# Optimization experiments

Hardware: AMD Instinct MI355X
Metric: run time of the kernel (lower is better)

Reference implementation:

```python
import jax, jax.numpy as jnp
import numpy as np

B = 256; L = 512; PRED = 96; DVARS = 21
P = 16; STRIDE = 16
N = (L - P) // STRIDE + 1      # 32 patches
DM = P * P                     # d_model = 256
K = 5                          # DctAtt low-freq coeffs
EPS_BN = 1e-5


def _dct_mats(n_len):
    # torch_dct DCT-II / DCT-III as dense matrices (exact same scaling as torch_dct)
    n = jnp.arange(n_len, dtype=jnp.float32)
    C = jnp.cos(jnp.pi * (2.0 * n[None, :] + 1.0) * n[:, None] / (2.0 * n_len))  # (k, m)
    D2 = 2.0 * C                                  # dct(x, norm=None):  X = x @ D2.T
    w0 = jnp.where(n == 0, 0.5, 1.0)
    D3 = (C.T * w0[None, :]) / n_len              # idct(X, norm=None): x = X @ D3.T
    rL = jnp.sqrt(jnp.asarray(n_len, jnp.float32))
    s_ortho = jnp.where(n == 0, 0.5 / rL, 0.5 * jnp.sqrt(2.0) / rL)  # unnorm -> ortho scale
    return D2, D3, s_ortho


def _bn(x, g, b):
    # BatchNorm1d, training-mode batch stats (biased var), x: (B, C, Lc)
    m = jnp.mean(x, axis=(0, 2), keepdims=True)
    v = jnp.var(x, axis=(0, 2), keepdims=True)
    return g[None, :, None] * (x - m) * jax.lax.rsqrt(v + EPS_BN) + b[None, :, None]


def _gelu(x):
    return jax.nn.gelu(x, approximate=False)  # torch nn.GELU default = exact erf


def setup_inputs():
    key = jax.random.key(0)
    ks = jax.random.split(key, 24)
    r = lambda i, shp, s=0.02: jax.random.normal(ks[i], shp, jnp.float32) * s
    return dict(
        x=jax.random.normal(ks[0], (B, L, DVARS), jnp.float32),
        w_dct=r(1, (DVARS,), 0.2), b_dct=r(2, (DVARS,), 0.02),
        W_embed=r(3, (P, DM), 0.05), b_embed=r(4, (DM,), 0.02),
        W_linres=r(5, (N * DM, PRED), 0.01), b_linres=r(6, (PRED,), 0.02),
        W_dres=r(7, (DM, P), 0.05), b_dres=r(8, (P,), 0.02),
        w_dc=r(9, (N, P), 0.1), b_dc=r(10, (N,), 0.02),
        w_dc1=r(11, (N, 3), 0.2), b_dc1=r(12, (N,), 0.02),
        g_dctnorm=jnp.ones((DVARS,), jnp.float32), b_dctnorm=jnp.zeros((DVARS,), jnp.float32),
        g_patchnorm=jnp.ones((N,), jnp.float32), b_patchnorm=jnp.zeros((N,), jnp.float32),
        g_depthnorm=jnp.ones((N,), jnp.float32), b_depthnorm=jnp.zeros((N,), jnp.float32),
        thr_p=jnp.array([0.3], jnp.float32),
        W_m1=r(13, (L, PRED), 0.02), b_m1=r(14, (PRED,), 0.02),
        W_m2=r(15, (PRED, PRED), 0.05), b_m2=r(16, (PRED,), 0.02),
        a_dw_w=r(17, (K,), 0.2), a_dw_b=r(18, (), 0.02),
        a_cw=jnp.float32(1.0) + r(19, (), 0.1), a_cb=r(20, (), 0.02),
        a_g=jnp.ones((), jnp.float32), a_b=jnp.zeros((), jnp.float32),
    )


def reference(x, w_dct, b_dct, W_embed, b_embed, W_linres, b_linres,
              W_dres, b_dres, w_dc, b_dc, w_dc1, b_dc1,
              g_dctnorm, b_dctnorm, g_patchnorm, b_patchnorm,
              g_depthnorm, b_depthnorm, thr_p,
              W_m1, b_m1, W_m2, b_m2,
              a_dw_w, a_dw_b, a_cw, a_cb, a_g, a_b):
    Bx = x.shape[0]
    D2, D3, s_ortho = _dct_mats(L)
    xT = jnp.transpose(x, (0, 2, 1))                       # (B,D,L)
    # dctConv = depthwise 1x1 conv => per-channel scale+bias (same layer reused twice)
    x_res = xT * w_dct[:, None] + b_dct[:, None]
    z_dct = xT @ D2.T                                      # dct(norm=None)
    # adaptive_high_freq_mask
    energy = jnp.sum(z_dct * z_dct, axis=-1)               # (B,D)
    med = jnp.median(energy, axis=1, keepdims=True)
    norm_e = energy / (med + 1e-6)
    thr = jnp.quantile(norm_e, thr_p[0])                   # global quantile over all elems
    mask = (norm_e > thr).astype(x.dtype)[..., None]       # broadcasts over freq axis
    z = (z_dct * mask) * w_dct[:, None] + b_dct[:, None]
    z = _gelu(z)
    z = _bn(z, g_dctnorm, b_dctnorm)
    z1 = z @ D3.T + x_res                                  # idct + residual, (B,D,L)
    # patchify (unfold)
    idx = jnp.arange(N)[:, None] * STRIDE + jnp.arange(P)[None, :]
    zp = xT[..., idx].reshape(Bx * DVARS, N, P)            # (BD,N,P)
    z_p = zp @ W_embed + b_embed                           # (BD,N,DM)
    z_res = jnp.transpose(z_p.reshape(Bx, DVARS, N * DM) @ W_linres + b_linres, (0, 2, 1))
    res = z_p @ W_dres + b_dres                            # (BD,N,P)
    # depth_conv: depthwise conv, kernel=P, stride=P over DM=P*P
    zd = jnp.einsum('bnqp,np->bnq', z_p.reshape(Bx * DVARS, N, P, P), w_dc) + b_dc[:, None]
    zd = _bn(zd + res, g_patchnorm, b_patchnorm)
    z2 = _gelu(zd)
    # depth_conv1: depthwise k=3 pad=1
    zpad = jnp.pad(z2, ((0, 0), (0, 0), (1, 1)))
    zc = (w_dc1[:, 0, None] * zpad[..., :-2] + w_dc1[:, 1, None] * zpad[..., 1:-1]
          + w_dc1[:, 2, None] * zpad[..., 2:]) + b_dc1[:, None]
    zc = _bn(zc, g_depthnorm, b_depthnorm)
    zc = _gelu(zc) + z2
    z2f = zc.reshape(Bx, DVARS, N * P)                     # (B,D,L)
    # DctAtt on z1*z2f (low-freq pick + dwConv(k=5,stride=5) + BN(1) + GELU + 1x1 + softmax)
    prod = z1 * z2f
    low = (prod @ D2.T[:, :K]) * s_ortho[:K]               # ortho DCT, first K coeffs (B,D,K)
    att = low @ a_dw_w + a_dw_b                            # (B,D)
    m = jnp.mean(att); v = jnp.var(att)
    att = a_g * (att - m) * jax.lax.rsqrt(v + EPS_BN) + a_b
    att = _gelu(att)
    att1 = jax.nn.softmax(att * a_cw + a_cb, axis=-1)[..., None]  # (B,D,1)
    zsum = z1 * att1 + z2f * (1.0 - att1)
    z_mlp = _gelu(zsum @ W_m1 + b_m1) @ W_m2 + b_m2        # Mlp, (B,D,PRED)
    return z_res + jnp.transpose(z_mlp, (0, 2, 1))         # (B,PRED,D)
```

## Files before the change

### kernel.cpp

```cpp
#include <hip/hip_runtime.h>
#include <hip/hip_bf16.h>

#define B_    256
#define L_    512
#define DV    21
#define NROW  5376
#define NP    32
#define PP    16
#define PRED_ 96

static const size_t OFF_XT    = 0;
static const size_t OFF_ZA    = 2752512;
static const size_t OFF_Z1    = 5505024;
static const size_t OFF_ZCP   = 8257536;
static const size_t OFF_D2    = 11010048;
static const size_t OFF_D3    = 11272192;
static const size_t OFF_M     = 11534336;
static const size_t OFF_TN    = 11583488;
static const size_t OFF_TB    = 11591680;
static const size_t OFF_C     = 11592192;
static const size_t OFF_EN    = 11592320;
static const size_t OFF_NORM  = 11597696;
static const size_t OFF_ATT   = 11603072;
static const size_t OFF_ATT1  = 11608448;
static const size_t OFF_STAT  = 11613824;
static const size_t OFF_ABD   = 11614080;
static const size_t OFF_ABP   = 11614144;
static const size_t OFF_ABDEP = 11614208;
static const size_t OFF_FLAG  = 11614272;
static const size_t OFF_STG   = 11614336;

static const int S_WDCT=0, S_BDCT=24, S_WE=48, S_BE=4144, S_WL=4400, S_BL=790832,
  S_WD=790928, S_BDRES=795024, S_WDC=795040, S_BDC=795552, S_WDC1=795584, S_BDC1=795680,
  S_GD=795712, S_BDN=795736, S_GP=795760, S_BP=795792, S_GDEP=795824, S_BDEP=795856,
  S_THR=795888, S_WM1=795892, S_BM1=845044, S_WM2=845140, S_BM2=854356,
  S_ADWW=854452, S_ADWB=854460, S_ACW=854464, S_ACB=854468, S_AG=854472, S_AB2=854476;

struct Ptrs { const void* p[30]; };

typedef __attribute__((ext_vector_type(8))) short bf16x8;
typedef __attribute__((ext_vector_type(4))) float f32x4;

__device__ __forceinline__ float bf2f(unsigned short h){
  unsigned u = ((unsigned)h) << 16;
  return __uint_as_float(u);
}
__device__ __forceinline__ short f2b(float f){
  unsigned u = __float_as_uint(f);
  u = (u + 0x7FFFu + ((u >> 16) & 1u)) >> 16;
  return (short)u;
}
__device__ __forceinline__ float gelu_f(float x){ return 0.5f*x*(1.0f+erff(x*0.70710678118654752440f)); }

__global__ void k_init(const unsigned* __restrict__ gones, float* __restrict__ stat,
                       float* __restrict__ c, float* __restrict__ M, int* __restrict__ flag){
  if (blockIdx.x == 0){
    stat[threadIdx.x] = 0.0f;
    if (threadIdx.x < 128) c[threadIdx.x] = 0.0f;
    if (threadIdx.x == 0) *flag = (gones[0] == 0x3F800000u) ? 1 : 0;
  } else {
    M[(blockIdx.x-1)*256 + threadIdx.x] = 0.0f;
  }
}

__global__ __launch_bounds__(256) void k_stage(Ptrs ptrs, float* __restrict__ dst, const int* __restrict__ flag){
  const int cnt[29] = {21,21,4096,256,786432,96,4096,16,512,32,96,32,21,21,32,32,32,32,1,49152,96,9216,96,5,1,1,1,1,1};
  const int off[29] = {S_WDCT,S_BDCT,S_WE,S_BE,S_WL,S_BL,S_WD,S_BDRES,S_WDC,S_BDC,S_WDC1,S_BDC1,
                       S_GD,S_BDN,S_GP,S_BP,S_GDEP,S_BDEP,S_THR,S_WM1,S_BM1,S_WM2,S_BM2,
                       S_ADWW,S_ADWB,S_ACW,S_ACB,S_AG,S_AB2};
  int mode = *flag;
  int gid = blockIdx.x*256 + threadIdx.x;
  int a = -1, loc = 0, base = 0;
  #pragma unroll
  for (int i = 0; i < 29; i++){
    if (a < 0 && gid < base + cnt[i]){ a = i; loc = gid - base; }
    base += cnt[i];
  }
  if (a < 0) return;
  const void* s = ptrs.p[a+1];
  float v = mode ? ((const float*)s)[loc] : bf2f(((const unsigned short*)s)[loc]);
  dst[off[a] + loc] = v;
}

__global__ __launch_bounds__(256) void k_transpose(const void* __restrict__ x, float* __restrict__ xt,
                                                   const int* __restrict__ flag){
  __shared__ float xs[128*DV];
  int mode = *flag;
  int b = blockIdx.x >> 2, ch = blockIdx.x & 3;
  int l0 = ch*128;
  size_t base = (size_t)b*(L_*DV) + (size_t)l0*DV;
  if (mode){
    const float* xp = (const float*)x + base;
    for (int i = threadIdx.x; i < 128*DV; i += 256) xs[i] = xp[i];
  } else {
    const unsigned short* xp = (const unsigned short*)x + base;
    for (int i = threadIdx.x; i < 128*DV; i += 256) xs[i] = bf2f(xp[i]);
  }
  __syncthreads();
  for (int i = threadIdx.x; i < 128*DV; i += 256){
    int d = i >> 7, l = i & 127;
    xt[((size_t)b*DV + d)*512 + l0 + l] = xs[l*DV + d];
  }
}

__global__ __launch_bounds__(256) void k_dctmats(float* __restrict__ D2, unsigned short* __restrict__ D3h){
  int i = blockIdx.x*256 + threadIdx.x;
  int kk = i >> 9, m = i & 511;
  const float PIo = 3.14159265358979323846f / 1024.0f;
  int a = ((2*m+1)*kk) & 2047;
  D2[i] = 2.0f * cosf(PIo * (float)a);
  int l = kk, k = m;
  int a2 = ((2*l+1)*k) & 2047;
  float w0 = (k==0) ? 0.5f : 1.0f;
  D3h[i] = (unsigned short)f2b(cosf(PIo * (float)a2) * w0 * (1.0f/512.0f));
}

__global__ void k_dvec(const float* __restrict__ S, float* __restrict__ dvec){
  int m = blockIdx.x*256 + threadIdx.x;
  const float PIo = 3.14159265358979323846f / 1024.0f;
  const float rs = 22.627416997969522f;
  float s = 0.f;
  #pragma unroll
  for (int k = 0; k < 5; k++){
    float sk = ((k == 0) ? 0.5f : 0.70710678118654752440f) / rs;
    int a = ((2*m+1)*k) & 2047;
    s += 2.0f * cosf(PIo * (float)a) * sk * S[S_ADWW + k];
  }
  dvec[m] = s;
}

__global__ __launch_bounds__(256) void k_foldM(const float* __restrict__ S, float* __restrict__ M){
  const float* We = S + S_WE;  const float* Wl = S + S_WL;
  int gid = blockIdx.x*256 + threadIdx.x;
  int l = gid/96, p = gid - l*96;
  int n = l>>4, q = l&15;
  int j0 = blockIdx.y*32;
  float acc = 0.f;
  #pragma unroll 8
  for (int j = j0; j < j0+32; j++) acc += We[q*256+j] * Wl[(size_t)(n*256+j)*96 + p];
  atomicAdd(&M[gid], acc);
}

__global__ __launch_bounds__(256) void k_foldC(const float* __restrict__ S, float* __restrict__ c){
  const float* be = S + S_BE;  const float* Wl = S + S_WL;  const float* bl = S + S_BL;
  int t = threadIdx.x;
  int rp = t >> 7, p = t & 127;
  if (p >= 96) return;
  float acc = 0.f;
  int J0 = blockIdx.x*64;
  for (int j = 0; j < 64; j += 2){
    int J = J0 + j + rp;
    acc += be[J & 255] * Wl[(size_t)J*96 + p];
  }
  if (blockIdx.x == 0 && rp == 0) acc += bl[p];
  atomicAdd(&c[p], acc);
}

__global__ __launch_bounds__(256) void k_foldTn(const float* __restrict__ S,
    float* __restrict__ Tn, float* __restrict__ tb){
  __shared__ float WeS[4096];
  __shared__ float WdS[4096];
  __shared__ float wdcS[16];
  __shared__ float beS[256];
  __shared__ float bdresS[16];
  int n = blockIdx.x, tid = threadIdx.x;
  for (int i = tid; i < 4096; i += 256){ WeS[i] = S[S_WE+i]; WdS[i] = S[S_WD+i]; }
  beS[tid & 255] = S[S_BE + (tid & 255)];
  if (tid < 16){ wdcS[tid] = S[S_WDC + n*16 + tid]; bdresS[tid] = S[S_BDRES + tid]; }
  __syncthreads();
  int q2 = tid>>4, q = tid&15;
  float R = 0.f;
  for (int j = 0; j < 256; j++) R += WeS[q2*256+j] * WdS[j*16+q];
  float G = 0.f;
  #pragma unroll
  for (int p = 0; p < 16; p++) G += WeS[q2*256 + q*16 + p] * wdcS[p];
  Tn[n*256 + q2*16 + q] = R + G;
  if (tid < 16){
    float rb = bdresS[tid];
    for (int j = 0; j < 256; j++) rb += beS[j] * WdS[j*16+tid];
    float gb = S[S_BDC + n];
    #pragma unroll
    for (int p = 0; p < 16; p++) gb += beS[tid*16+p] * wdcS[p];
    tb[n*16+tid] = rb + gb;
  }
}

__global__ __launch_bounds__(256) void k_gemm0(
    const float* __restrict__ A, const float* __restrict__ Bm, float* __restrict__ C){
  __shared__ float As[16][68];
  __shared__ float Bs[16][68];
  int tid = threadIdx.x;
  int tx = tid & 15, ty = tid >> 4;
  int rowBase = blockIdx.y * 64;
  int colBase = blockIdx.x * 64;
  int lr = tid >> 2;
  int lk = (tid & 3) << 2;
  float acc[4][4] = {};
  for (int k0 = 0; k0 < 512; k0 += 16){
    float4 av = *(const float4*)(A + (size_t)(rowBase+lr)*512 + k0 + lk);
    As[lk+0][lr] = av.x; As[lk+1][lr] = av.y; As[lk+2][lr] = av.z; As[lk+3][lr] = av.w;
    float4 bv = *(const float4*)(Bm + (size_t)(colBase+lr)*512 + k0 + lk);
    Bs[lk+0][lr] = bv.x; Bs[lk+1][lr] = bv.y; Bs[lk+2][lr] = bv.z; Bs[lk+3][lr] = bv.w;
    __syncthreads();
    #pragma unroll
    for (int kk = 0; kk < 16; kk++){
      float4 a4 = *(const float4*)&As[kk][ty*4];
      float4 b4 = *(const float4*)&Bs[kk][tx*4];
      acc[0][0] += a4.x*b4.x; acc[0][1] += a4.x*b4.y; acc[0][2] += a4.x*b4.z; acc[0][3] += a4.x*b4.w;
      acc[1][0] += a4.y*b4.x; acc[1][1] += a4.y*b4.y; acc[1][2] += a4.y*b4.z; acc[1][3] += a4.y*b4.w;
      acc[2][0] += a4.z*b4.x; acc[2][1] += a4.z*b4.y; acc[2][2] += a4.z*b4.z; acc[2][3] += a4.z*b4.w;
      acc[3][0] += a4.w*b4.x; acc[3][1] += a4.w*b4.y; acc[3][2] += a4.w*b4.z; acc[3][3] += a4.w*b4.w;
    }
    __syncthreads();
  }
  #pragma unroll
  for (int i = 0; i < 4; i++){
    int r = rowBase + ty*4 + i;
    #pragma unroll
    for (int j = 0; j < 4; j++){
      int cc = colBase + tx*4 + j;
      C[(size_t)r*512 + cc] = acc[i][j];
    }
  }
}

template<int MODE>
__global__ __launch_bounds__(256) void k_gemm_mf(
    const float* __restrict__ A, const float* __restrict__ A2,
    const unsigned short* __restrict__ Bg,
    float* __restrict__ C, const float* __restrict__ ab, const float* __restrict__ xt,
    const float* __restrict__ wdct, const float* __restrict__ bdct, int Cstride){
  __shared__ short Ah[64*40];
  __shared__ short Bh[64*40];
  int tid = threadIdx.x;
  int rowBase = blockIdx.y*64, colBase = blockIdx.x*64;
  int srow = tid>>2, seg = tid&3;
  int r = rowBase + srow;
  float alpha = 1.f, beta = 0.f;
  bool useXt = false;
  if (MODE == 1){ int d = r % DV; alpha = ab[2*d]; beta = ab[2*d+1]; }
  if (MODE == 3){ if (blockIdx.x < 2) alpha = ab[r]; else useXt = true; }
  int wave = tid>>6, lane = tid&63;
  int m = lane&15, quad = lane>>4;
  f32x4 acc[4] = {};
  const float* Ap = (MODE == 3 && useXt) ? xt : A;
  for (int k0 = 0; k0 < 512; k0 += 32){
    float4 a0 = *(const float4*)(Ap + (size_t)r*512 + k0 + seg*8);
    float4 a1 = *(const float4*)(Ap + (size_t)r*512 + k0 + seg*8 + 4);
    if (MODE == 1){
      a0.x = alpha*a0.x+beta; a0.y = alpha*a0.y+beta; a0.z = alpha*a0.z+beta; a0.w = alpha*a0.w+beta;
      a1.x = alpha*a1.x+beta; a1.y = alpha*a1.y+beta; a1.z = alpha*a1.z+beta; a1.w = alpha*a1.w+beta;
    }
    if (MODE == 3 && !useXt){
      float4 c0 = *(const float4*)(A2 + (size_t)r*512 + k0 + seg*8);
      float4 c1 = *(const float4*)(A2 + (size_t)r*512 + k0 + seg*8 + 4);
      float om = 1.0f - alpha;
      a0.x = alpha*a0.x + om*c0.x; a0.y = alpha*a0.y + om*c0.y;
      a0.z = alpha*a0.z + om*c0.z; a0.w = alpha*a0.w + om*c0.w;
      a1.x = alpha*a1.x + om*c1.x; a1.y = alpha*a1.y + om*c1.y;
      a1.z = alpha*a1.z + om*c1.z; a1.w = alpha*a1.w + om*c1.w;
    }
    bf16x8 av;
    av[0]=f2b(a0.x); av[1]=f2b(a0.y); av[2]=f2b(a0.z); av[3]=f2b(a0.w);
    av[4]=f2b(a1.x); av[5]=f2b(a1.y); av[6]=f2b(a1.z); av[7]=f2b(a1.w);
    *(bf16x8*)(Ah + srow*40 + seg*8) = av;
    bf16x8 bv = *(const bf16x8*)(Bg + (size_t)(colBase+srow)*512 + k0 + seg*8);
    *(bf16x8*)(Bh + srow*40 + seg*8) = bv;
    __syncthreads();
    bf16x8 af = *(bf16x8*)(Ah + (wave*16 + m)*40 + quad*8);
    #pragma unroll
    for (int t = 0; t < 4; t++){
      bf16x8 bf = *(bf16x8*)(Bh + (t*16 + m)*40 + quad*8);
      acc[t] = __builtin_amdgcn_mfma_f32_16x16x32_bf16(af, bf, acc[t], 0, 0, 0);
    }
    __syncthreads();
  }
  #pragma unroll
  for (int t = 0; t < 4; t++){
    #pragma unroll
    for (int i = 0; i < 4; i++){
      int rr = rowBase + wave*16 + quad*4 + i;
      int cc = colBase + t*16 + m;
      float v = acc[t][i];
      if (MODE == 1){
        int d = rr % DV;
        v += xt[(size_t)rr*512 + cc]*wdct[d] + bdct[d];
      }
      C[(size_t)rr*Cstride + cc] = v;
    }
  }
}

__global__ __launch_bounds__(256) void k_energy(const float* __restrict__ z, float* __restrict__ e){
  int tid = threadIdx.x;
  int r = blockIdx.x*4 + (tid>>6);
  int lane = tid & 63;
  const float* p = z + (size_t)r*512;
  float s = 0.f;
  #pragma unroll
  for (int w = 0; w < 8; w++){ float v = p[lane + w*64]; s += v*v; }
  for (int off = 32; off; off >>= 1) s += __shfl_down(s, off);
  if (lane == 0) e[r] = s;
}

__global__ __launch_bounds__(256) void k_med(const float* __restrict__ e, float* __restrict__ norm){
  int b = threadIdx.x;
  float v[DV];
  for (int d = 0; d < DV; d++) v[d] = e[b*DV + d];
  float med = 0.f;
  for (int i = 0; i < DV; i++){
    int rk = 0;
    for (int j = 0; j < DV; j++) rk += (v[j] < v[i]) || (v[j] == v[i] && j < i);
    if (rk == 10) med = v[i];
  }
  float den = med + 1e-6f;
  for (int d = 0; d < DV; d++) norm[b*DV + d] = v[d] / den;
}

__global__ __launch_bounds__(256) void k_rank(const float* __restrict__ norm,
    const float* __restrict__ thrv, float* __restrict__ stat){
  int tid = threadIdx.x;
  int cand = tid >> 4, part = tid & 15;
  int idx = blockIdx.x*16 + cand;
  float val = norm[idx];
  int cnt = 0;
  int j0 = part*336;
  for (int j = j0; j < j0 + 336; ++j){
    float v = norm[j];
    cnt += (v < val) || (v == val && j < idx);
  }
  __shared__ int sc[16][17];
  sc[cand][part] = cnt;
  __syncthreads();
  if (part == 0){
    int rank = 0;
    #pragma unroll
    for (int i = 0; i < 16; i++) rank += sc[cand][i];
    float q = thrv[0];
    float pos = q * 5375.0f;
    int i0 = (int)floorf(pos);
    int i1 = (i0 + 1 > 5375) ? 5375 : i0 + 1;
    if (rank == i0) stat[200] = val;
    if (rank == i1) stat[201] = val;
  }
}

__global__ __launch_bounds__(256) void k_maskgelu(float* __restrict__ zA, const float* __restrict__ norm,
    const float* __restrict__ stat, const float* __restrict__ thrv,
    const float* __restrict__ wdct, const float* __restrict__ bdct,
    float* __restrict__ part){
  int r = blockIdx.x, tid = threadIdx.x;
  int d = r % DV, brow = r / DV;
  float q = thrv[0];
  float pos = q * 5375.0f; float f = pos - floorf(pos);
  float thr = stat[200] + (stat[201] - stat[200]) * f;
  float mask = norm[r] > thr ? 1.0f : 0.0f;
  float w = wdct[d], b = bdct[d];
  float s = 0.f, s2 = 0.f;
  for (int i = tid; i < 512; i += 256){
    float v = zA[(size_t)r*512 + i] * mask * w + b;
    float g = gelu_f(v);
    zA[(size_t)r*512 + i] = g;
    s += g; s2 += g*g;
  }
  for (int off = 32; off; off >>= 1){ s += __shfl_down(s, off); s2 += __shfl_down(s2, off); }
  __shared__ float wsum[4][2];
  int wv = tid >> 6;
  if ((tid & 63) == 0){ wsum[wv][0] = s; wsum[wv][1] = s2; }
  __syncthreads();
  if (tid == 0){
    float S  = wsum[0][0]+wsum[1][0]+wsum[2][0]+wsum[3][0];
    float S2 = wsum[0][1]+wsum[1][1]+wsum[2][1]+wsum[3][1];
    part[(2*d)*256 + brow] = S;
    part[(2*d+1)*256 + brow] = S2;
  }
}

__global__ __launch_bounds__(256) void k_bnfin2(const float* __restrict__ part, int P,
    const float* __restrict__ g, const float* __restrict__ b, float count, float* __restrict__ ab){
  int c = blockIdx.x, tid = threadIdx.x;
  const float* ps = part + (size_t)(2*c)*P;
  const float* pq = part + (size_t)(2*c+1)*P;
  float s = 0.f, s2 = 0.f;
  for (int i = tid; i < P; i += 256){ s += ps[i]; s2 += pq[i]; }
  for (int off = 32; off; off >>= 1){ s += __shfl_down(s, off); s2 += __shfl_down(s2, off); }
  __shared__ float ws[4][2];
  if ((tid & 63) == 0){ ws[tid>>6][0] = s; ws[tid>>6][1] = s2; }
  __syncthreads();
  if (tid == 0){
    float S1 = ws[0][0]+ws[1][0]+ws[2][0]+ws[3][0];
    float S2 = ws[0][1]+ws[1][1]+ws[2][1]+ws[3][1];
    float mean = S1 / count;
    float var  = S2 / count - mean*mean;
    float al = g[c] * rsqrtf(var + 1e-5f);
    float be = b[c] - mean * al;
    ab[2*c] = al; ab[2*c+1] = be;
  }
}

__global__ __launch_bounds__(256) void k_patch(const float* __restrict__ xt, const float* __restrict__ Tn,
    const float* __restrict__ tb, float* __restrict__ t, float* __restrict__ part){
  int blk = blockIdx.x, tid = threadIdx.x;
  int n0 = tid >> 4, qq = tid & 15;
  int n1 = n0 + 16;
  float T0[16], T1[16];
  #pragma unroll
  for (int q2 = 0; q2 < 16; q2++){
    T0[q2] = Tn[n0*256 + q2*16 + qq];
    T1[q2] = Tn[n1*256 + q2*16 + qq];
  }
  float tb0 = tb[n0*16 + qq], tb1 = tb[n1*16 + qq];
  float s0 = 0.f, q0 = 0.f, s1 = 0.f, q1 = 0.f;
  #pragma unroll
  for (int rr = 0; rr < 4; rr++){
    int r = blk*4 + rr;
    float x0 = xt[(size_t)r*512 + tid];
    float x1 = xt[(size_t)r*512 + tid + 256];
    float a0 = tb0, a1 = tb1;
    #pragma unroll
    for (int q2 = 0; q2 < 16; q2++){
      a0 += __shfl(x0, q2, 16) * T0[q2];
      a1 += __shfl(x1, q2, 16) * T1[q2];
    }
    t[(size_t)r*512 + tid] = a0;       s0 += a0; q0 += a0*a0;
    t[(size_t)r*512 + tid + 256] = a1; s1 += a1; q1 += a1*a1;
  }
  #pragma unroll
  for (int off = 1; off < 16; off <<= 1){
    s0 += __shfl_xor(s0, off); q0 += __shfl_xor(q0, off);
    s1 += __shfl_xor(s1, off); q1 += __shfl_xor(q1, off);
  }
  if (qq == 0){
    part[(2*n0)*1344 + blk] = s0; part[(2*n0+1)*1344 + blk] = q0;
    part[(2*n1)*1344 + blk] = s1; part[(2*n1+1)*1344 + blk] = q1;
  }
}

__global__ __launch_bounds__(256) void k_z2(float* __restrict__ t, float* __restrict__ zcp,
    const float* __restrict__ abp, const float* __restrict__ wdc1,
    const float* __restrict__ bdc1, float* __restrict__ part){
  int blk = blockIdx.x, tid = threadIdx.x;
  int n0 = tid >> 4, qq = tid & 15;
  int n1 = n0 + 16;
  float al0 = abp[2*n0], be0 = abp[2*n0+1], al1 = abp[2*n1], be1 = abp[2*n1+1];
  float w00 = wdc1[n0*3], w01 = wdc1[n0*3+1], w02 = wdc1[n0*3+2], bb0 = bdc1[n0];
  float w10 = wdc1[n1*3], w11 = wdc1[n1*3+1], w12 = wdc1[n1*3+2], bb1 = bdc1[n1];
  float s0 = 0.f, q0 = 0.f, s1 = 0.f, q1 = 0.f;
  #pragma unroll
  for (int rr = 0; rr < 4; rr++){
    int r = blk*4 + rr;
    float v0 = t[(size_t)r*512 + tid];
    float v1 = t[(size_t)r*512 + tid + 256];
    float z0  = gelu_f(al0*v0 + be0);
    float z1v = gelu_f(al1*v1 + be1);
    float l0 = __shfl_up(z0, 1, 16);    if (qq == 0)  l0 = 0.f;
    float r0 = __shfl_down(z0, 1, 16);  if (qq == 15) r0 = 0.f;
    float l1 = __shfl_up(z1v, 1, 16);   if (qq == 0)  l1 = 0.f;
    float r1 = __shfl_down(z1v, 1, 16); if (qq == 15) r1 = 0.f;
    float cv0 = w00*l0 + w01*z0  + w02*r0 + bb0;
    float cv1 = w10*l1 + w11*z1v + w12*r1 + bb1;
    zcp[(size_t)r*512 + tid] = cv0;       t[(size_t)r*512 + tid] = z0;
    zcp[(size_t)r*512 + tid + 256] = cv1; t[(size_t)r*512 + tid + 256] = z1v;
    s0 += cv0; q0 += cv0*cv0; s1 += cv1; q1 += cv1*cv1;
  }
  #pragma unroll
  for (int off = 1; off < 16; off <<= 1){
    s0 += __shfl_xor(s0, off); q0 += __shfl_xor(q0, off);
    s1 += __shfl_xor(s1, off); q1 += __shfl_xor(q1, off);
  }
  if (qq == 0){
    part[(2*n0)*1344 + blk] = s0; part[(2*n0+1)*1344 + blk] = q0;
    part[(2*n1)*1344 + blk] = s1; part[(2*n1+1)*1344 + blk] = q1;
  }
}

__global__ __launch_bounds__(256) void k_z2fatt(float* __restrict__ zcp, const float* __restrict__ z2,
    const float* __restrict__ ab, const float* __restrict__ z1,
    const float* __restrict__ dvec, float* __restrict__ att){
  int r = blockIdx.x, tid = threadIdx.x;
  size_t base = (size_t)r*512;
  float s = 0.f;
  #pragma unroll
  for (int h = 0; h < 2; h++){
    int idx = tid + h*256;
    int n = (idx >> 4) & 31;
    float v = gelu_f(ab[2*n]*zcp[base+idx] + ab[2*n+1]) + z2[base+idx];
    zcp[base+idx] = v;
    s += z1[base+idx] * v * dvec[idx];
  }
  for (int off = 32; off; off >>= 1) s += __shfl_down(s, off);
  __shared__ float ws[4];
  if ((tid & 63) == 0) ws[tid>>6] = s;
  __syncthreads();
  if (tid == 0) att[r] = ws[0]+ws[1]+ws[2]+ws[3];
}

__global__ __launch_bounds__(256) void k_attfin(const float* __restrict__ att, const float* __restrict__ S,
                                                float* __restrict__ att1){
  __shared__ float ws[4][2];
  int tid = threadIdx.x;
  float s = 0.f, s2 = 0.f;
  for (int i = tid; i < NROW; i += 256){ float a = att[i]; s += a; s2 += a*a; }
  for (int off = 32; off; off >>= 1){ s += __shfl_down(s, off); s2 += __shfl_down(s2, off); }
  if ((tid & 63) == 0){ ws[tid>>6][0] = s; ws[tid>>6][1] = s2; }
  __syncthreads();
  float S1 = ws[0][0]+ws[1][0]+ws[2][0]+ws[3][0];
  float S2 = ws[0][1]+ws[1][1]+ws[2][1]+ws[3][1];
  float mean = S1 / 5376.0f;
  float var  = S2 / 5376.0f - mean*mean;
  float al = S[S_AG] * rsqrtf(var + 1e-5f);
  float bb = S[S_AB2];
  float cw = S[S_ACW], cb2 = S[S_ACB];
  int b = tid;
  float v[DV]; float mx = -1e30f;
  for (int d = 0; d < DV; d++){
    float a = att[b*DV + d];
    a = gelu_f(al*(a - mean) + bb);
    a = a*cw + cb2;
    v[d] = a; mx = fmaxf(mx, a);
  }
  float ss = 0.f;
  for (int d = 0; d < DV; d++){ v[d] = expf(v[d] - mx); ss += v[d]; }
  float inv = 1.0f / ss;
  for (int d = 0; d < DV; d++) att1[b*DV + d] = v[d] * inv;
}

__global__ __launch_bounds__(256) void k_bcat(const float* __restrict__ Wm1, const float* __restrict__ M,
                                              unsigned short* __restrict__ Bt){
  int i = blockIdx.x*256 + threadIdx.x;
  int c = i >> 9, m = i & 511;
  float v = 0.f;
  if (c < 96) v = Wm1[m*96 + c];
  else if (c >= 128 && c < 224) v = M[m*96 + (c - 128)];
  Bt[i] = (unsigned short)f2b(v);
}

__global__ __launch_bounds__(256) void k_out(const float* __restrict__ Hcat, const float* __restrict__ c,
    const float* __restrict__ S, void* __restrict__ outv, const int* __restrict__ flag){
  const float* bm1 = S + S_BM1;
  const float* Wm2 = S + S_WM2;
  const float* bm2 = S + S_BM2;
  __shared__ float W2s[96*96];
  __shared__ float Hs[16][100];
  int blk = blockIdx.x, tid = threadIdx.x;
  int r0 = blk*16;
  for (int i = tid; i < 96*96; i += 256) W2s[i] = Wm2[i];
  for (int i = tid; i < 16*96; i += 256){
    int rr = i / 96, col = i - rr*96;
    Hs[rr][col] = gelu_f(Hcat[(size_t)(r0+rr)*256 + col] + bm1[col]);
  }
  __syncthreads();
  int rr = tid >> 4, c0 = (tid & 15)*6;
  float acc[6] = {};
  for (int k = 0; k < 96; k++){
    float h = Hs[rr][k];
    #pragma unroll
    for (int j = 0; j < 6; j++) acc[j] += h * W2s[k*96 + c0 + j];
  }
  int r = r0 + rr;
  int b = r / DV, d = r - b*DV;
  int mode = *flag;
  #pragma unroll
  for (int j = 0; j < 6; j++){
    int p = c0 + j;
    float val = Hcat[(size_t)r*256 + 128 + p] + c[p] + acc[j] + bm2[p];
    size_t oi = ((size_t)b*96 + p)*DV + d;
    if (mode) ((float*)outv)[oi] = val;
    else ((__hip_bfloat16*)outv)[oi] = __float2bfloat16(val);
  }
}

extern "C" void kernel_launch(void* const* d_in, const int* in_sizes, int n_in,
                              void* d_out, int out_size, void* d_ws, size_t ws_size,
                              hipStream_t stream) {
  float* w = (float*)d_ws;
  float* xt   = w + OFF_XT;
  float* zA   = w + OFF_ZA;
  float* z1   = w + OFF_Z1;
  float* zcp  = w + OFF_ZCP;
  float* D2   = w + OFF_D2;
  unsigned short* D3h = (unsigned short*)(w + OFF_D3);
  float* Mb   = w + OFF_M;
  float* Tn   = w + OFF_TN;
  float* tb   = w + OFF_TB;
  float* cb   = w + OFF_C;
  float* en   = w + OFF_EN;
  float* nrm  = w + OFF_NORM;
  float* att  = w + OFF_ATT;
  float* att1 = w + OFF_ATT1;
  float* dvec = w + OFF_ATT1;
  float* stat = w + OFF_STAT;
  float* abd  = w + OFF_ABD;
  float* abp  = w + OFF_ABP;
  float* abdep= w + OFF_ABDEP;
  int*   flag = (int*)(w + OFF_FLAG);
  float* S    = w + OFF_STG;
  float* Hcat = zA;
  unsigned short* BcatTh = (unsigned short*)(zA + 1500000);
  float* partA = D2;
  float* partB = w + OFF_D3;

  Ptrs ptrs;
  for (int i = 0; i < 30; i++) ptrs.p[i] = d_in[i];

  k_init<<<193, 256, 0, stream>>>((const unsigned*)d_in[13], stat, cb, Mb, flag);
  k_stage<<<3338, 256, 0, stream>>>(ptrs, S, flag);
  k_transpose<<<1024, 256, 0, stream>>>(d_in[0], xt, flag);
  k_dctmats<<<1024, 256, 0, stream>>>(D2, D3h);
  k_dvec<<<2, 256, 0, stream>>>(S, dvec);
  k_foldM<<<dim3(192, 8), 256, 0, stream>>>(S, Mb);
  k_foldC<<<128, 256, 0, stream>>>(S, cb);
  k_foldTn<<<32, 256, 0, stream>>>(S, Tn, tb);

  k_gemm0<<<dim3(8,84), 256, 0, stream>>>(xt, D2, zA);
  k_energy<<<NROW/4, 256, 0, stream>>>(zA, en);
  k_med<<<1, 256, 0, stream>>>(en, nrm);
  k_rank<<<336, 256, 0, stream>>>(nrm, S+S_THR, stat);
  k_maskgelu<<<NROW, 256, 0, stream>>>(zA, nrm, stat, S+S_THR, S+S_WDCT, S+S_BDCT, partA);
  k_bnfin2<<<DV, 256, 0, stream>>>(partA, 256, S+S_GD, S+S_BDN, 131072.0f, abd);
  k_gemm_mf<1><<<dim3(8,84), 256, 0, stream>>>(zA, nullptr, D3h, z1, abd, xt, S+S_WDCT, S+S_BDCT, 512);

  k_patch<<<NROW/4, 256, 0, stream>>>(xt, Tn, tb, zA, partA);
  k_bnfin2<<<NP, 256, 0, stream>>>(partA, 1344, S+S_GP, S+S_BP, 86016.0f, abp);
  k_z2<<<NROW/4, 256, 0, stream>>>(zA, zcp, abp, S+S_WDC1, S+S_BDC1, partB);
  k_bnfin2<<<NP, 256, 0, stream>>>(partB, 1344, S+S_GDEP, S+S_BDEP, 86016.0f, abdep);
  k_z2fatt<<<NROW, 256, 0, stream>>>(zcp, zA, abdep, z1, dvec, att);
  k_attfin<<<1, 256, 0, stream>>>(att, S, att1);

  k_bcat<<<512, 256, 0, stream>>>(S+S_WM1, Mb, BcatTh);
  k_gemm_mf<3><<<dim3(4,84), 256, 0, stream>>>(z1, zcp, BcatTh, Hcat, att1, xt, nullptr, nullptr, 256);
  k_out<<<NROW/16, 256, 0, stream>>>(Hcat, cb, S, d_out, flag);
}
```

Baseline: 348.7 us.

## Run DCT GEMM on bf16 MFMA with hi/lo split and fuse energy reduction

The first DCT GEMM moves from an FP32 scalar-FMA tile loop to bf16 MFMA instructions. Both operands are split into hi and lo bf16 parts and multiplied with four MFMAs per tile to keep close to FP32 accuracy. The per-row energy sum-of-squares is now computed in the GEMM epilogue as per-block partials, reduced by a tiny kernel, which replaces the separate energy pass over zA. The dvec computation is folded into the DCT-matrix kernel to save a launch. The split-bf16 product drops the lo*lo rounding fidelity, so there is a small precision risk, and the workspace buffers are re-aliased.

```diff
diff --git a/kernel.cpp b/kernel.cpp
--- a/kernel.cpp
+++ b/kernel.cpp
@@ -103,30 +103,33 @@
   }
 }
 
-__global__ __launch_bounds__(256) void k_dctmats(float* __restrict__ D2, unsigned short* __restrict__ D3h){
+__global__ __launch_bounds__(256) void k_dctmats(unsigned short* __restrict__ D2h,
+    unsigned short* __restrict__ D2l, unsigned short* __restrict__ D3h,
+    const float* __restrict__ S, float* __restrict__ dvec){
   int i = blockIdx.x*256 + threadIdx.x;
   int kk = i >> 9, m = i & 511;
   const float PIo = 3.14159265358979323846f / 1024.0f;
   int a = ((2*m+1)*kk) & 2047;
-  D2[i] = 2.0f * cosf(PIo * (float)a);
+  float v = 2.0f * cosf(PIo * (float)a);
+  short hi = f2b(v);
+  float lo = v - bf2f((unsigned short)hi);
+  D2h[i] = (unsigned short)hi;
+  D2l[i] = (unsigned short)f2b(lo);
   int l = kk, k = m;
   int a2 = ((2*l+1)*k) & 2047;
   float w0 = (k==0) ? 0.5f : 1.0f;
   D3h[i] = (unsigned short)f2b(cosf(PIo * (float)a2) * w0 * (1.0f/512.0f));
-}
-
-__global__ void k_dvec(const float* __restrict__ S, float* __restrict__ dvec){
-  int m = blockIdx.x*256 + threadIdx.x;
-  const float PIo = 3.14159265358979323846f / 1024.0f;
-  const float rs = 22.627416997969522f;
-  float s = 0.f;
-  #pragma unroll
-  for (int k = 0; k < 5; k++){
-    float sk = ((k == 0) ? 0.5f : 0.70710678118654752440f) / rs;
-    int a = ((2*m+1)*k) & 2047;
-    s += 2.0f * cosf(PIo * (float)a) * sk * S[S_ADWW + k];
-  }
-  dvec[m] = s;
+  if (i < 512){
+    const float rs = 22.627416997969522f;
+    float s = 0.f;
+    #pragma unroll
+    for (int k5 = 0; k5 < 5; k5++){
+      float sk = ((k5 == 0) ? 0.5f : 0.70710678118654752440f) / rs;
+      int a5 = ((2*i+1)*k5) & 2047;
+      s += 2.0f * cosf(PIo * (float)a5) * sk * S[S_ADWW + k5];
+    }
+    dvec[i] = s;
+  }
 }
 
 __global__ __launch_bounds__(256) void k_foldM(const float* __restrict__ S, float* __restrict__ M){
@@ -186,42 +189,83 @@
 }
 
 __global__ __launch_bounds__(256) void k_gemm0(
-    const float* __restrict__ A, const float* __restrict__ Bm, float* __restrict__ C){
-  __shared__ float As[16][68];
-  __shared__ float Bs[16][68];
+    const float* __restrict__ A, const unsigned short* __restrict__ Bh16,
+    const unsigned short* __restrict__ Bl16, float* __restrict__ C,
+    float* __restrict__ e_part){
+  __shared__ short Ahi[64*40];
+  __shared__ short Alo[64*40];
+  __shared__ short Bhi[64*40];
+  __shared__ short Blo[64*40];
   int tid = threadIdx.x;
-  int tx = tid & 15, ty = tid >> 4;
-  int rowBase = blockIdx.y * 64;
-  int colBase = blockIdx.x * 64;
-  int lr = tid >> 2;
-  int lk = (tid & 3) << 2;
-  float acc[4][4] = {};
-  for (int k0 = 0; k0 < 512; k0 += 16){
-    float4 av = *(const float4*)(A + (size_t)(rowBase+lr)*512 + k0 + lk);
-    As[lk+0][lr] = av.x; As[lk+1][lr] = av.y; As[lk+2][lr] = av.z; As[lk+3][lr] = av.w;
-    float4 bv = *(const float4*)(Bm + (size_t)(colBase+lr)*512 + k0 + lk);
-    Bs[lk+0][lr] = bv.x; Bs[lk+1][lr] = bv.y; Bs[lk+2][lr] = bv.z; Bs[lk+3][lr] = bv.w;
+  int rowBase = blockIdx.y*64, colBase = blockIdx.x*64;
+  int srow = tid>>2, seg = tid&3;
+  int r = rowBase + srow;
+  int wave = tid>>6, lane = tid&63;
+  int m = lane&15, quad = lane>>4;
+  f32x4 acc[4] = {};
+  for (int k0 = 0; k0 < 512; k0 += 32){
+    float4 a0 = *(const float4*)(A + (size_t)r*512 + k0 + seg*8);
+    float4 a1 = *(const float4*)(A + (size_t)r*512 + k0 + seg*8 + 4);
+    bf16x8 ah, al;
+    {
+      float av[8] = {a0.x,a0.y,a0.z,a0.w,a1.x,a1.y,a1.z,a1.w};
+      #pragma unroll
+      for (int j = 0; j < 8; j++){
+        short h = f2b(av[j]);
+        ah[j] = h;
+        al[j] = f2b(av[j] - bf2f((unsigned short)h));
+      }
+    }
+    *(bf16x8*)(Ahi + srow*40 + seg*8) = ah;
+    *(bf16x8*)(Alo + srow*40 + seg*8) = al;
+    *(bf16x8*)(Bhi + srow*40 + seg*8) = *(const bf16x8*)(Bh16 + (size_t)(colBase+srow)*512 + k0 + seg*8);
+    *(bf16x8*)(Blo + srow*40 + seg*8) = *(const bf16x8*)(Bl16 + (size_t)(colBase+srow)*512 + k0 + seg*8);
     __syncthreads();
-    #pragma unroll
-    for (int kk = 0; kk < 16; kk++){
-      float4 a4 = *(const float4*)&As[kk][ty*4];
-      float4 b4 = *(const float4*)&Bs[kk][tx*4];
-      acc[0][0] += a4.x*b4.x; acc[0][1] += a4.x*b4.y; acc[0][2] += a4.x*b4.z; acc[0][3] += a4.x*b4.w;
-      acc[1][0] += a4.y*b4.x; acc[1][1] += a4.y*b4.y; acc[1][2] += a4.y*b4.z; acc[1][3] += a4.y*b4.w;
-      acc[2][0] += a4.z*b4.x; acc[2][1] += a4.z*b4.y; acc[2][2] += a4.z*b4.z; acc[2][3] += a4.z*b4.w;
-      acc[3][0] += a4.w*b4.x; acc[3][1] += a4.w*b4.y; acc[3][2] += a4.w*b4.z; acc[3][3] += a4.w*b4.w;
+    bf16x8 afh = *(bf16x8*)(Ahi + (wave*16 + m)*40 + quad*8);
+    bf16x8 afl = *(bf16x8*)(Alo + (wave*16 + m)*40 + quad*8);
+    #pragma unroll
+    for (int t = 0; t < 4; t++){
+      bf16x8 bfh = *(bf16x8*)(Bhi + (t*16 + m)*40 + quad*8);
+      bf16x8 bfl = *(bf16x8*)(Blo + (t*16 + m)*40 + quad*8);
+      acc[t] = __builtin_amdgcn_mfma_f32_16x16x32_bf16(afh, bfh, acc[t], 0, 0, 0);
+      acc[t] = __builtin_amdgcn_mfma_f32_16x16x32_bf16(afh, bfl, acc[t], 0, 0, 0);
+      acc[t] = __builtin_amdgcn_mfma_f32_16x16x32_bf16(afl, bfh, acc[t], 0, 0, 0);
+      acc[t] = __builtin_amdgcn_mfma_f32_16x16x32_bf16(afl, bfl, acc[t], 0, 0, 0);
     }
     __syncthreads();
   }
-  #pragma unroll
-  for (int i = 0; i < 4; i++){
-    int r = rowBase + ty*4 + i;
-    #pragma unroll
-    for (int j = 0; j < 4; j++){
-      int cc = colBase + tx*4 + j;
-      C[(size_t)r*512 + cc] = acc[i][j];
-    }
-  }
+  float es[4] = {};
+  #pragma unroll
+  for (int t = 0; t < 4; t++){
+    #pragma unroll
+    for (int i = 0; i < 4; i++){
+      int rr = rowBase + wave*16 + quad*4 + i;
+      int cc = colBase + t*16 + m;
+      float v = acc[t][i];
+      C[(size_t)rr*512 + cc] = v;
+      es[i] += v*v;
+    }
+  }
+  #pragma unroll
+  for (int off = 1; off < 16; off <<= 1){
+    #pragma unroll
+    for (int i = 0; i < 4; i++) es[i] += __shfl_xor(es[i], off);
+  }
+  if (m == 0){
+    #pragma unroll
+    for (int i = 0; i < 4; i++){
+      int rr = rowBase + wave*16 + quad*4 + i;
+      e_part[rr*8 + blockIdx.x] = es[i];
+    }
+  }
+}
+
+__global__ __launch_bounds__(256) void k_ered(const float* __restrict__ e_part, float* __restrict__ e){
+  int r = blockIdx.x*256 + threadIdx.x;
+  float s = 0.f;
+  #pragma unroll
+  for (int j = 0; j < 8; j++) s += e_part[r*8 + j];
+  e[r] = s;
 }
 
 template<int MODE>
@@ -291,18 +335,6 @@
   }
 }
 
-__global__ __launch_bounds__(256) void k_energy(const float* __restrict__ z, float* __restrict__ e){
-  int tid = threadIdx.x;
-  int r = blockIdx.x*4 + (tid>>6);
-  int lane = tid & 63;
-  const float* p = z + (size_t)r*512;
-  float s = 0.f;
-  #pragma unroll
-  for (int w = 0; w < 8; w++){ float v = p[lane + w*64]; s += v*v; }
-  for (int off = 32; off; off >>= 1) s += __shfl_down(s, off);
-  if (lane == 0) e[r] = s;
-}
-
 __global__ __launch_bounds__(256) void k_med(const float* __restrict__ e, float* __restrict__ norm){
   int b = threadIdx.x;
   float v[DV];
@@ -578,7 +610,8 @@
   float* zA   = w + OFF_ZA;
   float* z1   = w + OFF_Z1;
   float* zcp  = w + OFF_ZCP;
-  float* D2   = w + OFF_D2;
+  unsigned short* D2h = (unsigned short*)(w + OFF_D2);
+  unsigned short* D2l = (unsigned short*)(w + OFF_D2 + 131072);
   unsigned short* D3h = (unsigned short*)(w + OFF_D3);
   float* Mb   = w + OFF_M;
   float* Tn   = w + OFF_TN;
@@ -597,8 +630,9 @@
   float* S    = w + OFF_STG;
   float* Hcat = zA;
   unsigned short* BcatTh = (unsigned short*)(zA + 1500000);
-  float* partA = D2;
-  float* partB = w + OFF_D3;
+  float* partA  = w + OFF_D2;
+  float* e_part = w + OFF_D3 + 131072;
+  float* partB  = w + OFF_D3 + 131072;
 
   Ptrs ptrs;
   for (int i = 0; i < 30; i++) ptrs.p[i] = d_in[i];
@@ -606,14 +640,13 @@
   k_init<<<193, 256, 0, stream>>>((const unsigned*)d_in[13], stat, cb, Mb, flag);
   k_stage<<<3338, 256, 0, stream>>>(ptrs, S, flag);
   k_transpose<<<1024, 256, 0, stream>>>(d_in[0], xt, flag);
-  k_dctmats<<<1024, 256, 0, stream>>>(D2, D3h);
-  k_dvec<<<2, 256, 0, stream>>>(S, dvec);
+  k_dctmats<<<1024, 256, 0, stream>>>(D2h, D2l, D3h, S, dvec);
   k_foldM<<<dim3(192, 8), 256, 0, stream>>>(S, Mb);
   k_foldC<<<128, 256, 0, stream>>>(S, cb);
   k_foldTn<<<32, 256, 0, stream>>>(S, Tn, tb);
 
-  k_gemm0<<<dim3(8,84), 256, 0, stream>>>(xt, D2, zA);
-  k_energy<<<NROW/4, 256, 0, stream>>>(zA, en);
+  k_gemm0<<<dim3(8,84), 256, 0, stream>>>(xt, D2h, D2l, zA, e_part);
+  k_ered<<<21, 256, 0, stream>>>(e_part, en);
   k_med<<<1, 256, 0, stream>>>(en, nrm);
   k_rank<<<336, 256, 0, stream>>>(nrm, S+S_THR, stat);
   k_maskgelu<<<NROW, 256, 0, stream>>>(zA, nrm, stat, S+S_THR, S+S_WDCT, S+S_BDCT, partA);
```

Measured after the change: 318.9 us. 1.09x faster.
